# Kernel optimization log

Measured on AMD Instinct MI355X. Metric: run time of the kernel, lower is better.

Reference implementation:

```python
import jax, jax.numpy as jnp
import numpy as np

N_NODES = 100000
N_EDGES = 1600000
F_IN, F_HID, F_OUT = 128, 128, 40


def setup_inputs() -> dict:
    key = jax.random.key(0)
    ks = jax.random.split(key, 8)
    x = jax.random.normal(ks[0], (N_NODES, F_IN), dtype=jnp.float32)
    edge_index = jax.random.randint(ks[1], (2, N_EDGES), 0, N_NODES, dtype=jnp.int64)
    # GCNConv weights (glorot-style scale); biases zero per bias_init=zeros_
    W0 = jax.random.normal(ks[2], (F_IN, F_HID), dtype=jnp.float32) / np.sqrt(F_IN)
    b0 = jnp.zeros((F_HID,), dtype=jnp.float32)
    W1 = jax.random.normal(ks[3], (F_HID, F_HID), dtype=jnp.float32) / np.sqrt(F_HID)
    b1 = jnp.zeros((F_HID,), dtype=jnp.float32)
    W2 = jax.random.normal(ks[4], (F_HID, F_OUT), dtype=jnp.float32) / np.sqrt(F_HID)
    b2 = jnp.zeros((F_OUT,), dtype=jnp.float32)
    return {"x": x, "edge_index": edge_index, "W0": W0, "b0": b0,
            "W1": W1, "b1": b1, "W2": W2, "b2": b2}


def _gcn_conv(h, src, dst, W, b):
    # PyG GCNConv (normalize=False, add_self_loops=False):
    # linear transform, then sum-aggregate source features at destinations.
    h = h @ W                                   # [N, F_out]
    msgs = jnp.take(h, src, axis=0)             # [E, F_out] gather
    agg = jax.ops.segment_sum(msgs, dst, num_segments=N_NODES)  # scatter-add
    return agg + b


def reference(x, edge_index, W0, b0, W1, b1, W2, b2):
    src, dst = edge_index[0], edge_index[1]     # flow: source -> target
    h = jax.nn.relu(_gcn_conv(x, src, dst, W0, b0))
    h = jax.nn.relu(_gcn_conv(h, src, dst, W1, b1))
    out = _gcn_conv(h, src, dst, W2, b2)        # last layer: no activation
    return out
```

## Files before the change

kernel.cpp:

```cpp
#include <hip/hip_runtime.h>


typedef short bf16x8 __attribute__((ext_vector_type(8)));
typedef float f32x4  __attribute__((ext_vector_type(4)));

#define EPB 4096
#define P2CAP 6144

__device__ __forceinline__ float bflo(unsigned int v) {
  union { float f; unsigned int i; } w; w.i = v << 16; return w.f;
}
__device__ __forceinline__ float bfhi(unsigned int v) {
  union { float f; unsigned int i; } w; w.i = v & 0xffff0000u; return w.f;
}
__device__ __forceinline__ unsigned short f2bf(float f) {
  union { float f; unsigned int i; } w; w.f = f;
  unsigned int b = w.i;
  unsigned int r = (b + 0x7fffu + ((b >> 16) & 1u)) >> 16;
  return (unsigned short)r;
}

__device__ __forceinline__ int edge_at(const void* ei, int is64, long long pos) {
  if (is64) return (int)((const long long*)ei)[pos];
  return ((const int*)ei)[pos];
}

__device__ __forceinline__ void agg_accum(float* a, uint4 v) {
  a[0] += bflo(v.x); a[1] += bfhi(v.x);
  a[2] += bflo(v.y); a[3] += bfhi(v.y);
  a[4] += bflo(v.z); a[5] += bfhi(v.z);
  a[6] += bflo(v.w); a[7] += bfhi(v.w);
}

__global__ __launch_bounds__(256) void k_prep(const void* __restrict__ ei, int E,
                                              int* __restrict__ bhist,
                                              int NBKT, int NBLKE,
                                              const float* __restrict__ x,
                                              unsigned short* __restrict__ xb,
                                              long long n4, int ncvt,
                                              const float* __restrict__ W0,
                                              const float* __restrict__ W1,
                                              const float* __restrict__ W2,
                                              unsigned short* __restrict__ Wt0,
                                              unsigned short* __restrict__ Wt1,
                                              unsigned short* __restrict__ Wt2,
                                              unsigned short* __restrict__ bufH,
                                              unsigned short* __restrict__ t3,
                                              int FOUT, int N) {
  int blk = blockIdx.x, tid = threadIdx.x;
  if (blk < NBLKE) {
    __shared__ int h[512];
    __shared__ int s_is64;
    if (tid < 64) {
      int v = ((const int*)ei)[2 * tid + 1];
      unsigned long long m = __ballot(v != 0);
      if (tid == 0) s_is64 = (m == 0ull) ? 1 : 0;
    }
    for (int i = tid; i < NBKT; i += 256) h[i] = 0;
    __syncthreads();
    int is64 = s_is64;
    int base = blk * EPB;
    int cnt = min(EPB, E - base);
    for (int i = tid; i < cnt; i += 256) {
      int d = edge_at(ei, is64, (long long)E + base + i);
      atomicAdd(&h[d >> 8], 1);
    }
    __syncthreads();
    for (int i = tid; i < NBKT; i += 256) bhist[i * NBLKE + blk] = h[i];
  } else if (blk < NBLKE + ncvt) {
    long long i = (long long)(blk - NBLKE) * 256 + tid;
    if (i < n4) {
      float4 v = *reinterpret_cast<const float4*>(x + i * 4);
      ushort4 o;
      o.x = f2bf(v.x); o.y = f2bf(v.y); o.z = f2bf(v.z); o.w = f2bf(v.w);
      *reinterpret_cast<ushort4*>(xb + i * 4) = o;
    }
  } else {
    int idx = (blk - NBLKE - ncvt) * 256 + tid;
    if (idx < 16384) {
      int c = idx >> 7, k = idx & 127;
      Wt0[c * 128 + k] = f2bf(W0[k * 128 + c]);
    } else if (idx < 32768) {
      int t = idx - 16384;
      int c = t >> 7, k = t & 127;
      Wt1[c * 128 + k] = f2bf(W1[k * 128 + c]);
    } else if (idx < 40960) {
      int t = idx - 32768;
      int c = t >> 7, k = t & 127;
      Wt2[c * 128 + k] = (c < FOUT) ? f2bf(W2[k * FOUT + c]) : (unsigned short)0;
    } else if (idx < 41280) {
      int t = idx - 40960;
      if (t < 128)       xb[(size_t)N * 128 + t] = 0;
      else if (t < 256)  bufH[(size_t)N * 128 + (t - 128)] = 0;
      else               t3[(size_t)N * 64 + (t - 256)] = 0;
    }
  }
}

__global__ void k_scan_a(const int* __restrict__ vals, int* __restrict__ lscan,
                         int* __restrict__ partials, int n) {
  __shared__ int sm[256];
  int tid = threadIdx.x;
  int i = blockIdx.x * 256 + tid;
  int v = (i < n) ? vals[i] : 0;
  sm[tid] = v;
  __syncthreads();
  for (int off = 1; off < 256; off <<= 1) {
    int t = (tid >= off) ? sm[tid - off] : 0;
    __syncthreads();
    sm[tid] += t;
    __syncthreads();
  }
  if (i < n) lscan[i] = sm[tid];
  if (tid == 255) partials[blockIdx.x] = sm[255];
}

__global__ void k_scan_b(int* __restrict__ partials, int nb) {
  __shared__ int sm[1024];
  int tid = threadIdx.x;
  int i0 = 2 * tid, i1 = 2 * tid + 1;
  int v0 = (i0 < nb) ? partials[i0] : 0;
  int v1 = (i1 < nb) ? partials[i1] : 0;
  int s = v0 + v1;
  sm[tid] = s;
  __syncthreads();
  for (int off = 1; off < 1024; off <<= 1) {
    int t = (tid >= off) ? sm[tid - off] : 0;
    __syncthreads();
    sm[tid] += t;
    __syncthreads();
  }
  int excl = sm[tid] - s;
  if (i0 < nb) partials[i0] = excl;
  if (i1 < nb) partials[i1] = excl + v0;
}

__global__ void k_scan_c(const int* __restrict__ lscan, const int* __restrict__ vals,
                         const int* __restrict__ partials, int* __restrict__ scanned,
                         int* __restrict__ bucketPtr, int n, int NBLKE, int NBKT, int E) {
  int i = blockIdx.x * 256 + threadIdx.x;
  if (i >= n) return;
  int v = lscan[i] - vals[i] + partials[blockIdx.x];
  scanned[i] = v;
  int q = i / NBLKE;
  if (i - q * NBLKE == 0) bucketPtr[q] = v;
  if (i == 0) bucketPtr[NBKT] = E;
}

__global__ __launch_bounds__(256) void b_scatter(const void* __restrict__ ei, int E,
                                                 const int* __restrict__ scanned,
                                                 unsigned* __restrict__ ebuf,
                                                 int NBKT, int NBLKE) {
  __shared__ int base[512];
  __shared__ int s_is64;
  int blk = blockIdx.x, tid = threadIdx.x;
  if (tid < 64) {
    int v = ((const int*)ei)[2 * tid + 1];
    unsigned long long m = __ballot(v != 0);
    if (tid == 0) s_is64 = (m == 0ull) ? 1 : 0;
  }
  for (int i = tid; i < NBKT; i += 256) base[i] = scanned[i * NBLKE + blk];
  __syncthreads();
  int is64 = s_is64;
  int b0 = blk * EPB;
  int cnt = min(EPB, E - b0);
  for (int i = tid; i < cnt; i += 256) {
    int d = edge_at(ei, is64, (long long)E + b0 + i);
    int s = edge_at(ei, is64, b0 + i);
    int pos = atomicAdd(&base[d >> 8], 1);
    ebuf[pos] = (unsigned)s | ((unsigned)(d & 255) << 24);
  }
}

__global__ __launch_bounds__(256) void b_pass2(const unsigned* __restrict__ ebuf,
                                               const int* __restrict__ bucketPtr,
                                               int* __restrict__ rowptr,
                                               int* __restrict__ colsrc,
                                               int N, int NBKT, int E) {
  __shared__ int hist[256], excl[256], cur[256], sm[256];
  __shared__ int stage[P2CAP];
  int b = blockIdx.x, tid = threadIdx.x;
  hist[tid] = 0;
  __syncthreads();
  int beg = bucketPtr[b], end = bucketPtr[b + 1];
  int cnt = end - beg;
  for (int i = beg + tid; i < end; i += 256)
    atomicAdd(&hist[ebuf[i] >> 24], 1);
  __syncthreads();
  int v = hist[tid];
  sm[tid] = v;
  __syncthreads();
  for (int off = 1; off < 256; off <<= 1) {
    int t = (tid >= off) ? sm[tid - off] : 0;
    __syncthreads();
    sm[tid] += t;
    __syncthreads();
  }
  excl[tid] = sm[tid] - v;
  cur[tid] = 0;
  __syncthreads();
  int nb0 = b << 8;
  if (nb0 + tid < N) rowptr[nb0 + tid] = beg + excl[tid];
  if (b == 0 && tid == 0) rowptr[N] = E;
  bool st = (cnt <= P2CAP);
  for (int i = beg + tid; i < end; i += 256) {
    unsigned e2 = ebuf[i];
    int dl = (int)(e2 >> 24);
    int r = atomicAdd(&cur[dl], 1);
    int pos = excl[dl] + r;
    int val = (int)(e2 & 0xFFFFFFu);
    if (st) stage[pos] = val;
    else    colsrc[beg + pos] = val;
  }
  __syncthreads();
  if (st) {
    for (int i = tid; i < cnt; i += 256) colsrc[beg + i] = stage[i];
  }
}

__global__ __launch_bounds__(256, 8) void k_agg128b(
    const char* __restrict__ Hb,
    const int* __restrict__ rowptr, const int* __restrict__ colsrc,
    unsigned int* __restrict__ out, int N) {
  int node = blockIdx.x * 4 + (threadIdx.x >> 6);
  if (node >= N) return;
  int l = threadIdx.x & 63, sub = l >> 4, fl = l & 15;
  int beg = rowptr[node], end = rowptr[node + 1];
  int nb = (end - beg + 15) >> 4;
  const unsigned zoff = (unsigned)N << 8;
  unsigned flo = (unsigned)fl * 16u;
  float a[8] = {0.f, 0.f, 0.f, 0.f, 0.f, 0.f, 0.f, 0.f};
  for (int t = 0; t < nb; ++t) {
    int e = beg + t * 16 + sub * 4;
    int em = end - 1;
    int i0 = e, i1 = e + 1, i2 = e + 2, i3 = e + 3;
    int s0 = colsrc[i0 < end ? i0 : em];
    int s1 = colsrc[i1 < end ? i1 : em];
    int s2 = colsrc[i2 < end ? i2 : em];
    int s3 = colsrc[i3 < end ? i3 : em];
    unsigned o0 = (i0 < end ? ((unsigned)s0 << 8) : zoff) + flo;
    unsigned o1 = (i1 < end ? ((unsigned)s1 << 8) : zoff) + flo;
    unsigned o2 = (i2 < end ? ((unsigned)s2 << 8) : zoff) + flo;
    unsigned o3 = (i3 < end ? ((unsigned)s3 << 8) : zoff) + flo;
    uint4 v0 = *reinterpret_cast<const uint4*>(Hb + o0);
    uint4 v1 = *reinterpret_cast<const uint4*>(Hb + o1);
    uint4 v2 = *reinterpret_cast<const uint4*>(Hb + o2);
    uint4 v3 = *reinterpret_cast<const uint4*>(Hb + o3);
    agg_accum(a, v0); agg_accum(a, v1); agg_accum(a, v2); agg_accum(a, v3);
  }
  #pragma unroll
  for (int k = 0; k < 8; ++k) {
    a[k] += __shfl_xor(a[k], 16);
    a[k] += __shfl_xor(a[k], 32);
  }
  if (sub == 0) {
    uint4 o;
    o.x = ((unsigned)f2bf(a[1]) << 16) | f2bf(a[0]);
    o.y = ((unsigned)f2bf(a[3]) << 16) | f2bf(a[2]);
    o.z = ((unsigned)f2bf(a[5]) << 16) | f2bf(a[4]);
    o.w = ((unsigned)f2bf(a[7]) << 16) | f2bf(a[6]);
    *reinterpret_cast<uint4*>(out + (size_t)node * 64 + fl * 4) = o;
  }
}

__global__ __launch_bounds__(256, 8) void k_agg40(
    const char* __restrict__ Tb,
    const int* __restrict__ rowptr, const int* __restrict__ colsrc,
    const float* __restrict__ b2, float* __restrict__ out, int N) {
  int node = blockIdx.x * 4 + (threadIdx.x >> 6);
  if (node >= N) return;
  int l = threadIdx.x & 63, sub = l >> 4, fl = l & 15;
  int beg = rowptr[node], end = rowptr[node + 1];
  int nb = (end - beg + 15) >> 4;
  const unsigned zoff = (unsigned)N << 7;
  unsigned flo = (unsigned)fl * 8u;
  float a[4] = {0.f, 0.f, 0.f, 0.f};
  if (fl < 10) {
    for (int t = 0; t < nb; ++t) {
      int e = beg + t * 16 + sub * 4;
      int em = end - 1;
      int i0 = e, i1 = e + 1, i2 = e + 2, i3 = e + 3;
      int s0 = colsrc[i0 < end ? i0 : em];
      int s1 = colsrc[i1 < end ? i1 : em];
      int s2 = colsrc[i2 < end ? i2 : em];
      int s3 = colsrc[i3 < end ? i3 : em];
      unsigned o0 = (i0 < end ? ((unsigned)s0 << 7) : zoff) + flo;
      unsigned o1 = (i1 < end ? ((unsigned)s1 << 7) : zoff) + flo;
      unsigned o2 = (i2 < end ? ((unsigned)s2 << 7) : zoff) + flo;
      unsigned o3 = (i3 < end ? ((unsigned)s3 << 7) : zoff) + flo;
      uint2 v0 = *reinterpret_cast<const uint2*>(Tb + o0);
      uint2 v1 = *reinterpret_cast<const uint2*>(Tb + o1);
      uint2 v2 = *reinterpret_cast<const uint2*>(Tb + o2);
      uint2 v3 = *reinterpret_cast<const uint2*>(Tb + o3);
      a[0] += (bflo(v0.x) + bflo(v1.x)) + (bflo(v2.x) + bflo(v3.x));
      a[1] += (bfhi(v0.x) + bfhi(v1.x)) + (bfhi(v2.x) + bfhi(v3.x));
      a[2] += (bflo(v0.y) + bflo(v1.y)) + (bflo(v2.y) + bflo(v3.y));
      a[3] += (bfhi(v0.y) + bfhi(v1.y)) + (bfhi(v2.y) + bfhi(v3.y));
    }
  }
  #pragma unroll
  for (int k = 0; k < 4; ++k) {
    a[k] += __shfl_xor(a[k], 16);
    a[k] += __shfl_xor(a[k], 32);
  }
  if (sub == 0 && fl < 10) {
    float4 o;
    o.x = a[0] + b2[fl * 4 + 0];
    o.y = a[1] + b2[fl * 4 + 1];
    o.z = a[2] + b2[fl * 4 + 2];
    o.w = a[3] + b2[fl * 4 + 3];
    *reinterpret_cast<float4*>(out + (size_t)node * 40 + fl * 4) = o;
  }
}

template <int CHAIN>
__global__ __launch_bounds__(256) void k_gemm(const unsigned short* __restrict__ A,
                                              const unsigned short* __restrict__ Wt,
                                              const float* __restrict__ bias,
                                              const unsigned short* __restrict__ Wt2,
                                              unsigned short* __restrict__ C, int N) {
  __shared__ unsigned short sh16[CHAIN ? 4 * 2048 : 64];
  int tid = threadIdx.x;
  int w = tid >> 6, l = tid & 63;
  int sub = l >> 4, fl = l & 15;
  int r0 = blockIdx.x * 64 + w * 16;
  int arow = r0 + fl;
  if (arow >= N) arow = N - 1;
  int kk = sub * 8;
  bf16x8 af[4];
  #pragma unroll
  for (int ks = 0; ks < 4; ++ks)
    af[ks] = *reinterpret_cast<const bf16x8*>(A + (size_t)arow * 128 + ks * 32 + kk);

  int ccol = fl;
  int crow0 = r0 + sub * 4;

  if (CHAIN == 0) {
    #pragma unroll
    for (int cf = 0; cf < 8; ++cf) {
      f32x4 acc = {0.f, 0.f, 0.f, 0.f};
      const unsigned short* wp = Wt + (size_t)(cf * 16 + ccol) * 128 + kk;
      #pragma unroll
      for (int ks = 0; ks < 4; ++ks) {
        bf16x8 b = *reinterpret_cast<const bf16x8*>(wp + ks * 32);
        acc = __builtin_amdgcn_mfma_f32_16x16x32_bf16(af[ks], b, acc, 0, 0, 0);
      }
      float bv = bias[cf * 16 + ccol];
      #pragma unroll
      for (int r = 0; r < 4; ++r) {
        int gr = crow0 + r;
        if (gr < N)
          C[(size_t)gr * 128 + cf * 16 + ccol] = f2bf(fmaxf(acc[r] + bv, 0.f));
      }
    }
  } else {
    unsigned short* my = &sh16[w * 2048];
    #pragma unroll
    for (int cf = 0; cf < 8; ++cf) {
      f32x4 acc = {0.f, 0.f, 0.f, 0.f};
      const unsigned short* wp = Wt + (size_t)(cf * 16 + ccol) * 128 + kk;
      #pragma unroll
      for (int ks = 0; ks < 4; ++ks) {
        bf16x8 b = *reinterpret_cast<const bf16x8*>(wp + ks * 32);
        acc = __builtin_amdgcn_mfma_f32_16x16x32_bf16(af[ks], b, acc, 0, 0, 0);
      }
      float bv = bias[cf * 16 + ccol];
      int col = cf * 16 + ccol;
      int chunk = col >> 3;
      #pragma unroll
      for (int r = 0; r < 4; ++r) {
        int row = sub * 4 + r;
        my[row * 128 + ((chunk ^ row) << 3) + (col & 7)] = f2bf(fmaxf(acc[r] + bv, 0.f));
      }
    }
    bf16x8 af3[4];
    #pragma unroll
    for (int ks = 0; ks < 4; ++ks) {
      int c = ks * 4 + sub;
      af3[ks] = *reinterpret_cast<const bf16x8*>(&my[fl * 128 + ((c ^ fl) << 3)]);
    }
    #pragma unroll
    for (int cf = 0; cf < 4; ++cf) {
      f32x4 acc = {0.f, 0.f, 0.f, 0.f};
      const unsigned short* wp = Wt2 + (size_t)(cf * 16 + ccol) * 128 + kk;
      #pragma unroll
      for (int ks = 0; ks < 4; ++ks) {
        bf16x8 b = *reinterpret_cast<const bf16x8*>(wp + ks * 32);
        acc = __builtin_amdgcn_mfma_f32_16x16x32_bf16(af3[ks], b, acc, 0, 0, 0);
      }
      #pragma unroll
      for (int r = 0; r < 4; ++r) {
        int gr = crow0 + r;
        if (gr < N)
          C[(size_t)gr * 64 + cf * 16 + ccol] = f2bf(acc[r]);
      }
    }
  }
}

extern "C" void kernel_launch(void* const* d_in, const int* in_sizes, int n_in,
                              void* d_out, int out_size, void* d_ws, size_t ws_size,
                              hipStream_t stream) {
  const float* x  = (const float*)d_in[0];
  const void*  ei = d_in[1];
  const float* W0 = (const float*)d_in[2];
  const float* b0 = (const float*)d_in[3];
  const float* W1 = (const float*)d_in[4];
  const float* b1 = (const float*)d_in[5];
  const float* W2 = (const float*)d_in[6];
  const float* b2 = (const float*)d_in[7];
  float* out = (float*)d_out;

  const int N = in_sizes[0] / 128;
  const int E = in_sizes[1] / 2;
  const int FOUT = in_sizes[6] / 128;

  const int NBLKE = (E + EPB - 1) / EPB;
  const int NBKT  = (N + 255) / 256;
  const int T     = NBKT * NBLKE;
  const int GS    = (T + 255) / 256;

  char* wp = (char*)d_ws;
  auto alloc = [&](size_t bytes) -> void* {
    void* p = (void*)wp;
    wp += (bytes + 255) & ~(size_t)255;
    return p;
  };
  unsigned short* xb   = (unsigned short*)alloc((size_t)(N + 1) * 128 * 2);
  unsigned short* bufA = (unsigned short*)alloc((size_t)N * 128 * 2);
  unsigned short* bufH = (unsigned short*)alloc((size_t)(N + 1) * 128 * 2);
  unsigned short* t3   = (unsigned short*)alloc((size_t)(N + 1) * 64 * 2);
  unsigned short* Wt0  = (unsigned short*)alloc(128 * 128 * 2);
  unsigned short* Wt1  = (unsigned short*)alloc(128 * 128 * 2);
  unsigned short* Wt2  = (unsigned short*)alloc(64 * 128 * 2);
  unsigned* ebuf = (unsigned*)alloc((size_t)E * 4);
  int* colsrc   = (int*)alloc((size_t)E * 4);
  int* rowptr   = (int*)alloc((size_t)(N + 1) * 4);
  int* bhist    = (int*)alloc((size_t)T * 4);
  int* lscan    = (int*)alloc((size_t)T * 4);
  int* scanned  = (int*)alloc((size_t)T * 4);
  int* partials = (int*)alloc(8192);
  int* bucketPtr= (int*)alloc((size_t)(NBKT + 1) * 4);

  long long n4 = (long long)N * 32;
  int ncvt = (int)((n4 + 255) / 256);
  int nwt  = (40960 + 320 + 255) / 256;

  k_prep<<<NBLKE + ncvt + nwt, 256, 0, stream>>>(ei, E, bhist, NBKT, NBLKE,
                                                 x, xb, n4, ncvt,
                                                 W0, W1, W2, Wt0, Wt1, Wt2,
                                                 bufH, t3, FOUT, N);
  k_scan_a<<<GS, 256, 0, stream>>>(bhist, lscan, partials, T);
  k_scan_b<<<1, 1024, 0, stream>>>(partials, GS);
  k_scan_c<<<GS, 256, 0, stream>>>(lscan, bhist, partials, scanned, bucketPtr,
                                   T, NBLKE, NBKT, E);
  b_scatter<<<NBLKE, 256, 0, stream>>>(ei, E, scanned, ebuf, NBKT, NBLKE);
  b_pass2<<<NBKT, 256, 0, stream>>>(ebuf, bucketPtr, rowptr, colsrc, N, NBKT, E);

  int gagg = (N + 3) / 4;
  int ggemm = (N + 63) / 64;
  k_agg128b<<<gagg, 256, 0, stream>>>((const char*)xb, rowptr, colsrc,
                                      (unsigned int*)bufA, N);
  k_gemm<0><<<ggemm, 256, 0, stream>>>(bufA, Wt0, b0, nullptr, bufH, N);
  k_agg128b<<<gagg, 256, 0, stream>>>((const char*)bufH, rowptr, colsrc,
                                      (unsigned int*)bufA, N);
  k_gemm<1><<<ggemm, 256, 0, stream>>>(bufA, Wt1, b1, Wt2, t3, N);
  k_agg40<<<gagg, 256, 0, stream>>>((const char*)t3, rowptr, colsrc, b2, out, N);
}
```

Baseline: 277.6 us.

## Fuse three-kernel scan into one with last-block decoupled partial scan

Replaces the three scan kernels with a single kernel in which the last block to finish, detected via an atomic counter reset in k_prep, scans the block partials. The final scanned offsets and bucket pointers are no longer materialized; consumers recompute them on the fly from lscan, bhist and partials. This removes two kernel launches and one pass over the scan array, at the cost of extra loads in the scatter and pass2 kernels and a serialized tail in the last scan block.

Result: slower. 314.4 us (+13.3%).

```diff
diff --git a/kernel.cpp b/kernel.cpp
--- a/kernel.cpp
+++ b/kernel.cpp
@@ -46,6 +46,7 @@
                                               unsigned short* __restrict__ Wt2,
                                               unsigned short* __restrict__ bufH,
                                               unsigned short* __restrict__ t3,
+                                              int* __restrict__ done,
                                               int FOUT, int N) {
   int blk = blockIdx.x, tid = threadIdx.x;
   if (blk < NBLKE) {
@@ -93,13 +94,20 @@
       if (t < 128)       xb[(size_t)N * 128 + t] = 0;
       else if (t < 256)  bufH[(size_t)N * 128 + (t - 128)] = 0;
       else               t3[(size_t)N * 64 + (t - 256)] = 0;
-    }
-  }
-}
-
-__global__ void k_scan_a(const int* __restrict__ vals, int* __restrict__ lscan,
-                         int* __restrict__ partials, int n) {
+    } else if (idx == 41280) {
+      *done = 0;
+    }
+  }
+}
+
+__global__ __launch_bounds__(256) void k_scanA(const int* __restrict__ vals,
+                                               int* __restrict__ lscan,
+                                               int* __restrict__ partials,
+                                               int* __restrict__ done,
+                                               int n, int GS) {
   __shared__ int sm[256];
+  __shared__ int tsum[256];
+  __shared__ int isLast;
   int tid = threadIdx.x;
   int i = blockIdx.x * 256 + tid;
   int v = (i < n) ? vals[i] : 0;
@@ -113,42 +121,50 @@
   }
   if (i < n) lscan[i] = sm[tid];
   if (tid == 255) partials[blockIdx.x] = sm[255];
-}
-
-__global__ void k_scan_b(int* __restrict__ partials, int nb) {
-  __shared__ int sm[1024];
-  int tid = threadIdx.x;
-  int i0 = 2 * tid, i1 = 2 * tid + 1;
-  int v0 = (i0 < nb) ? partials[i0] : 0;
-  int v1 = (i1 < nb) ? partials[i1] : 0;
-  int s = v0 + v1;
-  sm[tid] = s;
-  __syncthreads();
-  for (int off = 1; off < 1024; off <<= 1) {
-    int t = (tid >= off) ? sm[tid - off] : 0;
-    __syncthreads();
-    sm[tid] += t;
-    __syncthreads();
-  }
-  int excl = sm[tid] - s;
-  if (i0 < nb) partials[i0] = excl;
-  if (i1 < nb) partials[i1] = excl + v0;
-}
-
-__global__ void k_scan_c(const int* __restrict__ lscan, const int* __restrict__ vals,
-                         const int* __restrict__ partials, int* __restrict__ scanned,
-                         int* __restrict__ bucketPtr, int n, int NBLKE, int NBKT, int E) {
-  int i = blockIdx.x * 256 + threadIdx.x;
-  if (i >= n) return;
-  int v = lscan[i] - vals[i] + partials[blockIdx.x];
-  scanned[i] = v;
-  int q = i / NBLKE;
-  if (i - q * NBLKE == 0) bucketPtr[q] = v;
-  if (i == 0) bucketPtr[NBKT] = E;
+  __threadfence();
+  __syncthreads();
+  if (tid == 0) {
+    int old = atomicAdd(done, 1);
+    isLast = (old == GS - 1) ? 1 : 0;
+  }
+  __syncthreads();
+  if (!isLast) return;
+  __threadfence();
+  int loc[8];
+  int base = tid * 8;
+  int s = 0;
+  #pragma unroll
+  for (int j = 0; j < 8; ++j) {
+    int idx = base + j;
+    int pv = (idx < GS) ? partials[idx] : 0;
+    loc[j] = s;
+    s += pv;
+  }
+  tsum[tid] = s;
+  __syncthreads();
+  for (int off = 1; off < 256; off <<= 1) {
+    int t = (tid >= off) ? tsum[tid - off] : 0;
+    __syncthreads();
+    tsum[tid] += t;
+    __syncthreads();
+  }
+  int texcl = tsum[tid] - s;
+  #pragma unroll
+  for (int j = 0; j < 8; ++j) {
+    int idx = base + j;
+    if (idx < GS) partials[idx] = texcl + loc[j];
+  }
+}
+
+__device__ __forceinline__ int scanned_at(const int* lscan, const int* vals,
+                                          const int* partials, int g) {
+  return lscan[g] - vals[g] + partials[g >> 8];
 }
 
 __global__ __launch_bounds__(256) void b_scatter(const void* __restrict__ ei, int E,
-                                                 const int* __restrict__ scanned,
+                                                 const int* __restrict__ lscan,
+                                                 const int* __restrict__ vals,
+                                                 const int* __restrict__ partials,
                                                  unsigned* __restrict__ ebuf,
                                                  int NBKT, int NBLKE) {
   __shared__ int base[512];
@@ -159,7 +175,10 @@
     unsigned long long m = __ballot(v != 0);
     if (tid == 0) s_is64 = (m == 0ull) ? 1 : 0;
   }
-  for (int i = tid; i < NBKT; i += 256) base[i] = scanned[i * NBLKE + blk];
+  for (int i = tid; i < NBKT; i += 256) {
+    int g = i * NBLKE + blk;
+    base[i] = scanned_at(lscan, vals, partials, g);
+  }
   __syncthreads();
   int is64 = s_is64;
   int b0 = blk * EPB;
@@ -173,16 +192,23 @@
 }
 
 __global__ __launch_bounds__(256) void b_pass2(const unsigned* __restrict__ ebuf,
-                                               const int* __restrict__ bucketPtr,
+                                               const int* __restrict__ lscan,
+                                               const int* __restrict__ vals,
+                                               const int* __restrict__ partials,
                                                int* __restrict__ rowptr,
                                                int* __restrict__ colsrc,
-                                               int N, int NBKT, int E) {
+                                               int N, int NBKT, int NBLKE, int E) {
   __shared__ int hist[256], excl[256], cur[256], sm[256];
   __shared__ int stage[P2CAP];
+  __shared__ int s_beg, s_end;
   int b = blockIdx.x, tid = threadIdx.x;
   hist[tid] = 0;
-  __syncthreads();
-  int beg = bucketPtr[b], end = bucketPtr[b + 1];
+  if (tid == 0) {
+    s_beg = scanned_at(lscan, vals, partials, b * NBLKE);
+    s_end = (b + 1 < NBKT) ? scanned_at(lscan, vals, partials, (b + 1) * NBLKE) : E;
+  }
+  __syncthreads();
+  int beg = s_beg, end = s_end;
   int cnt = end - beg;
   for (int i = beg + tid; i < end; i += 256)
     atomicAdd(&hist[ebuf[i] >> 24], 1);
@@ -438,24 +464,22 @@
   int* rowptr   = (int*)alloc((size_t)(N + 1) * 4);
   int* bhist    = (int*)alloc((size_t)T * 4);
   int* lscan    = (int*)alloc((size_t)T * 4);
-  int* scanned  = (int*)alloc((size_t)T * 4);
   int* partials = (int*)alloc(8192);
-  int* bucketPtr= (int*)alloc((size_t)(NBKT + 1) * 4);
+  int* done     = (int*)alloc(256);
 
   long long n4 = (long long)N * 32;
   int ncvt = (int)((n4 + 255) / 256);
-  int nwt  = (40960 + 320 + 255) / 256;
+  int nwt  = (41536 + 255) / 256;
 
   k_prep<<<NBLKE + ncvt + nwt, 256, 0, stream>>>(ei, E, bhist, NBKT, NBLKE,
                                                  x, xb, n4, ncvt,
                                                  W0, W1, W2, Wt0, Wt1, Wt2,
-                                                 bufH, t3, FOUT, N);
-  k_scan_a<<<GS, 256, 0, stream>>>(bhist, lscan, partials, T);
-  k_scan_b<<<1, 1024, 0, stream>>>(partials, GS);
-  k_scan_c<<<GS, 256, 0, stream>>>(lscan, bhist, partials, scanned, bucketPtr,
-                                   T, NBLKE, NBKT, E);
-  b_scatter<<<NBLKE, 256, 0, stream>>>(ei, E, scanned, ebuf, NBKT, NBLKE);
-  b_pass2<<<NBKT, 256, 0, stream>>>(ebuf, bucketPtr, rowptr, colsrc, N, NBKT, E);
+                                                 bufH, t3, done, FOUT, N);
+  k_scanA<<<GS, 256, 0, stream>>>(bhist, lscan, partials, done, T, GS);
+  b_scatter<<<NBLKE, 256, 0, stream>>>(ei, E, lscan, bhist, partials, ebuf,
+                                       NBKT, NBLKE);
+  b_pass2<<<NBKT, 256, 0, stream>>>(ebuf, lscan, bhist, partials, rowptr, colsrc,
+                                    N, NBKT, NBLKE, E);
 
   int gagg = (N + 3) / 4;
   int ggemm = (N + 63) / 64;
```
